# Kernel tuning notes

Measured on AMD Instinct MI355X. Metric: run time of the kernel, lower is better.

The kernel has to match this reference:

```python
import jax, jax.numpy as jnp
import numpy as np

N_NODES = 40000
N_EDGES = 160000
N_FEATS = 74
H, D = 3, 1024
NODES_PER_GRAPH = 50
N_GRAPHS = N_NODES // NODES_PER_GRAPH


def setup_inputs() -> dict:
    key = jax.random.key(0)
    ks = jax.random.split(key, 12)
    inp = {
        "feats": jax.random.normal(ks[0], (N_NODES, N_FEATS), jnp.float32),
        "W": jax.random.normal(ks[1], (N_FEATS, H * D), jnp.float32) * 0.05,
        "attn_l": jax.random.normal(ks[2], (H, D), jnp.float32) * 0.05,
        "attn_r": jax.random.normal(ks[3], (H, D), jnp.float32) * 0.05,
        "bias_gat": jax.random.normal(ks[4], (H * D,), jnp.float32) * 0.05,
        "W1": jax.random.normal(ks[5], (H * D, D), jnp.float32) * 0.02,
        "b1": jax.random.normal(ks[6], (D,), jnp.float32) * 0.02,
        "W2": jax.random.normal(ks[7], (D, 1), jnp.float32) * 0.02,
        "b2": jax.random.normal(ks[8], (1,), jnp.float32) * 0.02,
        "src": jax.random.randint(ks[9], (N_EDGES,), 0, N_NODES, jnp.int32),
        "dst": jax.random.randint(ks[10], (N_EDGES,), 0, N_NODES, jnp.int32),
        "graph_ids": (jnp.arange(N_NODES, dtype=jnp.int32) // NODES_PER_GRAPH),
        "n_graphs": N_GRAPHS,
    }
    return inp


def reference(feats, W, attn_l, attn_r, bias_gat, W1, b1, W2, b2, src, dst, graph_ids, n_graphs):
    N = feats.shape[0]
    # --- DGL GATConv ---
    h = (feats @ W).reshape(N, H, D)                       # [N,H,D]
    el = jnp.sum(h * attn_l, axis=-1)                      # [N,H]
    er = jnp.sum(h * attn_r, axis=-1)                      # [N,H]
    e = jax.nn.leaky_relu(el[src] + er[dst], 0.2)          # [E,H] per-edge logits
    # edge softmax over incoming edges of each dst node
    m = jax.ops.segment_max(e, dst, num_segments=N)        # [N,H]
    ex = jnp.exp(e - m[dst])
    s = jax.ops.segment_sum(ex, dst, num_segments=N)       # [N,H]
    alpha = ex / s[dst]                                    # [E,H]
    msg = h[src] * alpha[..., None]                        # [E,H,D]
    out = jax.ops.segment_sum(msg, dst, num_segments=N)    # [N,H,D]
    out = out + bias_gat.reshape(H, D)
    # --- flatten + linear + LeakyReLU(True) (negative_slope=1.0 -> identity) ---
    x = out.reshape(N, H * D) @ W1 + b1                    # [N,D]
    # --- AvgPooling over each graph ---
    counts = jax.ops.segment_sum(jnp.ones((N,), x.dtype), graph_ids, num_segments=n_graphs)
    g = jax.ops.segment_sum(x, graph_ids, num_segments=n_graphs) / jnp.maximum(counts, 1.0)[:, None]
    y = g @ W2 + b2                                        # [n_graphs,1]
    return y
```

## Files before the change

### kernel.cpp

```cpp
#include <hip/hip_runtime.h>

#define N_NODES 40000
#define N_EDGES 160000
#define N_FEATS 74
#define DD 1024
#define HD 3072
#define N_GRAPHS 800

#define NVB 192
#define NTB 57
#define NCH 64
#define ECH (N_EDGES / NCH)
#define SNR 200
#define SRNG 200
#define NNB 313

__device__ __forceinline__ float waveReduceSum(float v) {
    #pragma unroll
    for (int off = 32; off > 0; off >>= 1)
        v += __shfl_down(v, off, 64);
    return v;
}
__device__ __forceinline__ float lrelu02(float x) { return x > 0.f ? x : 0.2f * x; }

__global__ __launch_bounds__(256) void kVFusedC(
    const float* __restrict__ W1, const float* __restrict__ W2,
    const float* __restrict__ b1, const float* __restrict__ b2,
    const float* __restrict__ W, const float* __restrict__ al,
    const float* __restrict__ ar, const float* __restrict__ bias,
    const int* __restrict__ dst,
    float* __restrict__ c0, float* __restrict__ bgvpar,
    float* __restrict__ wvpar, float* __restrict__ lw6,
    int* __restrict__ counts_c) {
    int wave = threadIdx.x >> 6, lane = threadIdx.x & 63;
    int tid = threadIdx.x;
    if (blockIdx.x < NVB) {
        __shared__ float vs[16];
        int b = blockIdx.x;
        int g0 = b * 16;
        int h = b >> 6;
        const float4* w2v = (const float4*)W2;
        #pragma unroll
        for (int q = 0; q < 4; ++q) {
            int g = g0 + wave * 4 + q;
            const float4* row = (const float4*)(W1 + (size_t)g * DD);
            float acc = 0.f;
            #pragma unroll
            for (int k = 0; k < 4; ++k) {
                float4 a = row[lane + 64 * k];
                float4 bb = w2v[lane + 64 * k];
                acc += a.x * bb.x + a.y * bb.y + a.z * bb.z + a.w * bb.w;
            }
            acc = waveReduceSum(acc);
            if (!lane) vs[wave * 4 + q] = acc;
        }
        __syncthreads();
        if (tid < N_FEATS) {
            const float4* wr = (const float4*)(W + (size_t)tid * HD + g0);
            const float4* vv = (const float4*)vs;
            float s = 0.f;
            #pragma unroll
            for (int k = 0; k < 4; ++k) {
                float4 a = wr[k];
                float4 bb = vv[k];
                s += a.x * bb.x + a.y * bb.y + a.z * bb.z + a.w * bb.w;
            }
            wvpar[((size_t)(h * N_FEATS + tid)) * 64 + (b & 63)] = s;
        } else if (tid == N_FEATS) {
            float s = 0.f;
            #pragma unroll
            for (int j = 0; j < 16; ++j) s += vs[j] * bias[g0 + j];
            bgvpar[b] = s;
        }
    } else if (blockIdx.x < NVB + NTB) {
        int t = (blockIdx.x - NVB) * 4 + wave;
        if (t < N_FEATS * 3) {
            int f = t / 3, h = t - f * 3;
            const float4* rw = (const float4*)(W + (size_t)f * HD + h * DD);
            const float4* pl = (const float4*)(al + h * DD);
            const float4* pr = (const float4*)(ar + h * DD);
            float aL = 0.f, aR = 0.f;
            #pragma unroll
            for (int k = 0; k < 4; ++k) {
                float4 x = rw[lane + 64 * k];
                float4 l4 = pl[lane + 64 * k];
                float4 r4 = pr[lane + 64 * k];
                aL += x.x * l4.x + x.y * l4.y + x.z * l4.z + x.w * l4.w;
                aR += x.x * r4.x + x.y * r4.y + x.z * r4.z + x.w * r4.w;
            }
            aL = waveReduceSum(aL); aR = waveReduceSum(aR);
            if (!lane) { lw6[f * 6 + h] = aL; lw6[f * 6 + 3 + h] = aR; }
        } else if (t == N_FEATS * 3) {
            const float4* pb1 = (const float4*)b1;
            const float4* w2v = (const float4*)W2;
            float acc = 0.f;
            #pragma unroll
            for (int k = 0; k < 4; ++k) {
                float4 a = pb1[lane + 64 * k];
                float4 bb = w2v[lane + 64 * k];
                acc += a.x * bb.x + a.y * bb.y + a.z * bb.z + a.w * bb.w;
            }
            acc = waveReduceSum(acc);
            if (!lane) c0[0] = acc + b2[0];
        }
    } else {
        __shared__ int hist[SNR];
        int cc = blockIdx.x - (NVB + NTB);
        for (int i = tid; i < SNR; i += 256) hist[i] = 0;
        __syncthreads();
        const int eb = cc * ECH;
        for (int i = tid; i < ECH; i += 256) {
            int d = dst[eb + i];
            atomicAdd(&hist[d / SRNG], 1);
        }
        __syncthreads();
        for (int i = tid; i < SNR; i += 256) counts_c[cc * SNR + i] = hist[i];
    }
}

__global__ __launch_bounds__(256) void kNodeScatter(const float* __restrict__ feats,
        const int* __restrict__ dst,
        const float* __restrict__ lw6, const float* __restrict__ wvpar,
        const int* __restrict__ counts_c,
        float4* __restrict__ sn4, float4* __restrict__ er4,
        int* __restrict__ ebuf) {
    int tid = threadIdx.x;
    if (blockIdx.x < NNB) {
        __shared__ float lw[N_FEATS * 9];
        for (int j = tid; j < 222 * 4; j += 256) {
            int g4 = j >> 2, sl = j & 3;
            int h = g4 / N_FEATS, f = g4 - h * N_FEATS;
            const float* p = wvpar + (size_t)g4 * 64 + sl * 16;
            float s = 0.f;
            #pragma unroll
            for (int k = 0; k < 16; ++k) s += p[k];
            s += __shfl_xor(s, 1, 64);
            s += __shfl_xor(s, 2, 64);
            if (!sl) lw[f * 9 + 6 + h] = s;
        }
        for (int i = tid; i < N_FEATS * 6; i += 256)
            lw[(i / 6) * 9 + (i % 6)] = lw6[i];
        __syncthreads();
        int node = blockIdx.x * 128 + (tid >> 1);
        if (node >= N_NODES) return;
        int half = tid & 1;
        const float* row = feats + (size_t)node * N_FEATS;
        float a0=0,a1=0,a2=0,a3=0,a4=0,a5=0,a6=0,a7=0,a8=0;
        if (half == 0) {
            #pragma unroll
            for (int k = 0; k < 18; ++k) {
                float2 x2 = *(const float2*)(row + k * 2);
                const float* w0 = lw + (k * 2) * 9;
                a0 += x2.x*w0[0]; a1 += x2.x*w0[1]; a2 += x2.x*w0[2];
                a3 += x2.x*w0[3]; a4 += x2.x*w0[4]; a5 += x2.x*w0[5];
                a6 += x2.x*w0[6]; a7 += x2.x*w0[7]; a8 += x2.x*w0[8];
                const float* w1 = w0 + 9;
                a0 += x2.y*w1[0]; a1 += x2.y*w1[1]; a2 += x2.y*w1[2];
                a3 += x2.y*w1[3]; a4 += x2.y*w1[4]; a5 += x2.y*w1[5];
                a6 += x2.y*w1[6]; a7 += x2.y*w1[7]; a8 += x2.y*w1[8];
            }
            float x = row[36];
            const float* wp = lw + 36 * 9;
            a0 += x*wp[0]; a1 += x*wp[1]; a2 += x*wp[2];
            a3 += x*wp[3]; a4 += x*wp[4]; a5 += x*wp[5];
            a6 += x*wp[6]; a7 += x*wp[7]; a8 += x*wp[8];
        } else {
            float x = row[37];
            const float* wp = lw + 37 * 9;
            a0 += x*wp[0]; a1 += x*wp[1]; a2 += x*wp[2];
            a3 += x*wp[3]; a4 += x*wp[4]; a5 += x*wp[5];
            a6 += x*wp[6]; a7 += x*wp[7]; a8 += x*wp[8];
            #pragma unroll
            for (int k = 0; k < 18; ++k) {
                float2 x2 = *(const float2*)(row + 38 + k * 2);
                const float* w0 = lw + (38 + k * 2) * 9;
                a0 += x2.x*w0[0]; a1 += x2.x*w0[1]; a2 += x2.x*w0[2];
                a3 += x2.x*w0[3]; a4 += x2.x*w0[4]; a5 += x2.x*w0[5];
                a6 += x2.x*w0[6]; a7 += x2.x*w0[7]; a8 += x2.x*w0[8];
                const float* w1 = w0 + 9;
                a0 += x2.y*w1[0]; a1 += x2.y*w1[1]; a2 += x2.y*w1[2];
                a3 += x2.y*w1[3]; a4 += x2.y*w1[4]; a5 += x2.y*w1[5];
                a6 += x2.y*w1[6]; a7 += x2.y*w1[7]; a8 += x2.y*w1[8];
            }
        }
        a0 += __shfl_xor(a0, 1, 64); a1 += __shfl_xor(a1, 1, 64);
        a2 += __shfl_xor(a2, 1, 64); a3 += __shfl_xor(a3, 1, 64);
        a4 += __shfl_xor(a4, 1, 64); a5 += __shfl_xor(a5, 1, 64);
        a6 += __shfl_xor(a6, 1, 64); a7 += __shfl_xor(a7, 1, 64);
        a8 += __shfl_xor(a8, 1, 64);
        if (!half) {
            sn4[node * 2]     = make_float4(a0, a1, a2, 0.f);
            sn4[node * 2 + 1] = make_float4(a6, a7, a8, 0.f);
            er4[node]         = make_float4(a3, a4, a5, 0.f);
        }
    } else {
        __shared__ int tot[SNR], myoff[SNR], cursor[SNR], baseP[SNR];
        int c = blockIdx.x - NNB;
        if (tid < SNR) {
            int t = 0, mo = 0;
            #pragma unroll 8
            for (int cc = 0; cc < NCH; ++cc) {
                int v = counts_c[cc * SNR + tid];
                t += v;
                if (cc < c) mo += v;
            }
            tot[tid] = t; myoff[tid] = mo;
        }
        __syncthreads();
        if (tid == 0) {
            int b = 0;
            for (int r = 0; r < SNR; ++r) { baseP[r] = b; b += tot[r]; }
        }
        __syncthreads();
        if (tid < SNR) cursor[tid] = baseP[tid] + myoff[tid];
        __syncthreads();
        const int eb = c * ECH;
        for (int i = tid; i < ECH; i += 256) {
            int e = eb + i;
            int d = dst[e];
            int r = d / SRNG;
            int rr = d - r * SRNG;
            int slot = atomicAdd(&cursor[r], 1);
            ebuf[slot] = (e << 8) | rr;
        }
    }
}

__global__ __launch_bounds__(1024) void kProcess(const int* __restrict__ src,
        const int* __restrict__ ebuf, const int* __restrict__ counts_c,
        const float4* __restrict__ sn4, const float4* __restrict__ er4,
        const float* __restrict__ bgvpar, const float* __restrict__ c0,
        float* __restrict__ y) {
    __shared__ float erL[SRNG * 4];
    __shared__ float acc[SRNG * 6];
    __shared__ int tot[SNR];
    __shared__ int baseS[2];
    int tid = threadIdx.x, wave = tid >> 6, lane = tid & 63;
    const int r = blockIdx.x;
    if (tid < SNR) {
        int s = 0;
        #pragma unroll 8
        for (int cc = 0; cc < NCH; ++cc) s += counts_c[cc * SNR + tid];
        tot[tid] = s;
    }
    for (int i = tid; i < SRNG * 6; i += 1024) acc[i] = 0.f;
    if (tid < SRNG) ((float4*)erL)[tid] = er4[(size_t)r * SRNG + tid];
    __syncthreads();
    if (tid == 0) {
        int b = 0;
        for (int q = 0; q < SNR; ++q) { if (q == r) baseS[0] = b; b += tot[q]; }
        baseS[1] = baseS[0] + tot[r];
    }
    __syncthreads();
    int b0 = baseS[0], b1 = baseS[1];
    for (int i = b0 + tid; i < b1; i += 1024) {
        int pk = ebuf[i];
        int rr = pk & 255;
        int e  = ((unsigned)pk) >> 8;
        int s  = src[e];
        float4 L = sn4[s * 2];
        float4 V = sn4[s * 2 + 1];
        const float* R = erL + rr * 4;
        float e0 = expf(lrelu02(L.x + R[0]));
        float e1 = expf(lrelu02(L.y + R[1]));
        float e2 = expf(lrelu02(L.z + R[2]));
        float* p = acc + rr * 6;
        atomicAdd(p + 0, e0 * V.x);
        atomicAdd(p + 1, e1 * V.y);
        atomicAdd(p + 2, e2 * V.z);
        atomicAdd(p + 3, e0);
        atomicAdd(p + 4, e1);
        atomicAdd(p + 5, e2);
    }
    __syncthreads();
    if (wave < 4) {
        float b = 0.f;
        for (int i = lane; i < NVB; i += 64) b += bgvpar[i];
        b = waveReduceSum(b);
        float cacc = 0.f;
        if (lane < 50) {
            const float* p = acc + (wave * 50 + lane) * 6;
            if (p[3] > 0.f) cacc = p[0] / p[3] + p[1] / p[4] + p[2] / p[5];
        }
        cacc = waveReduceSum(cacc);
        if (!lane) y[r * 4 + wave] = cacc * (1.f / 50.f) + b + c0[0];
    }
}

extern "C" void kernel_launch(void* const* d_in, const int* in_sizes, int n_in,
                              void* d_out, int out_size, void* d_ws, size_t ws_size,
                              hipStream_t stream) {
    const float* feats = (const float*)d_in[0];
    const float* W     = (const float*)d_in[1];
    const float* al    = (const float*)d_in[2];
    const float* ar    = (const float*)d_in[3];
    const float* bias  = (const float*)d_in[4];
    const float* W1    = (const float*)d_in[5];
    const float* b1    = (const float*)d_in[6];
    const float* W2    = (const float*)d_in[7];
    const float* b2    = (const float*)d_in[8];
    const int*   src   = (const int*)d_in[9];
    const int*   dst   = (const int*)d_in[10];

    float* ws      = (float*)d_ws;
    float* lw6     = ws;
    float* c0      = ws + 448;
    float* bgvpar  = ws + 512;
    float* wvpar   = ws + 1024;
    int*   countsc = (int*)(ws + 16384);
    int*   ebuf    = (int*)(ws + 32768);
    float* sn      = ws + 196608;
    float* er      = ws + 516608;
    float* y       = (float*)d_out;

    hipLaunchKernelGGL(kVFusedC, dim3(NVB + NTB + NCH), dim3(256), 0, stream,
                       W1, W2, b1, b2, W, al, ar, bias, dst,
                       c0, bgvpar, wvpar, lw6, countsc);
    hipLaunchKernelGGL(kNodeScatter, dim3(NNB + NCH), dim3(256), 0, stream,
                       feats, dst, lw6, wvpar, countsc,
                       (float4*)sn, (float4*)er, ebuf);
    hipLaunchKernelGGL(kProcess, dim3(SNR), dim3(1024), 0, stream,
                       src, ebuf, countsc, (const float4*)sn, (const float4*)er,
                       bgvpar, c0, y);
}
```

Measured before the change: 41.03 us.

## Bucket edges in one pass using fixed-capacity per-chunk slots

The separate histogram pass and the prefix-sum scatter pass are replaced by a single pass. Each edge chunk writes its edges straight into a fixed-capacity slot (CAP entries) per (dst range, chunk) and records per-chunk counts. The node-projection kernel no longer carries scatter blocks. The processing kernel builds a 64-entry prefix over chunk counts and binary-searches it to locate each edge. This removes one read of dst and the cross-chunk offset computation, at the cost of sparser ebuf reads and an assumption that no bucket exceeds CAP entries.

```diff
diff --git a/kernel.cpp b/kernel.cpp
--- a/kernel.cpp
+++ b/kernel.cpp
@@ -11,6 +11,7 @@
 #define NTB 57
 #define NCH 64
 #define ECH (N_EDGES / NCH)
+#define CAP 96
 #define SNR 200
 #define SRNG 200
 #define NNB 313
@@ -23,7 +24,7 @@
 }
 __device__ __forceinline__ float lrelu02(float x) { return x > 0.f ? x : 0.2f * x; }
 
-__global__ __launch_bounds__(256) void kVFusedC(
+__global__ __launch_bounds__(256) void kPre(
     const float* __restrict__ W1, const float* __restrict__ W2,
     const float* __restrict__ b1, const float* __restrict__ b2,
     const float* __restrict__ W, const float* __restrict__ al,
@@ -31,7 +32,7 @@
     const int* __restrict__ dst,
     float* __restrict__ c0, float* __restrict__ bgvpar,
     float* __restrict__ wvpar, float* __restrict__ lw6,
-    int* __restrict__ counts_c) {
+    int* __restrict__ cnt, int* __restrict__ ebuf) {
     int wave = threadIdx.x >> 6, lane = threadIdx.x & 63;
     int tid = threadIdx.x;
     if (blockIdx.x < NVB) {
@@ -104,115 +105,9 @@
             if (!lane) c0[0] = acc + b2[0];
         }
     } else {
-        __shared__ int hist[SNR];
-        int cc = blockIdx.x - (NVB + NTB);
-        for (int i = tid; i < SNR; i += 256) hist[i] = 0;
-        __syncthreads();
-        const int eb = cc * ECH;
-        for (int i = tid; i < ECH; i += 256) {
-            int d = dst[eb + i];
-            atomicAdd(&hist[d / SRNG], 1);
-        }
-        __syncthreads();
-        for (int i = tid; i < SNR; i += 256) counts_c[cc * SNR + i] = hist[i];
-    }
-}
-
-__global__ __launch_bounds__(256) void kNodeScatter(const float* __restrict__ feats,
-        const int* __restrict__ dst,
-        const float* __restrict__ lw6, const float* __restrict__ wvpar,
-        const int* __restrict__ counts_c,
-        float4* __restrict__ sn4, float4* __restrict__ er4,
-        int* __restrict__ ebuf) {
-    int tid = threadIdx.x;
-    if (blockIdx.x < NNB) {
-        __shared__ float lw[N_FEATS * 9];
-        for (int j = tid; j < 222 * 4; j += 256) {
-            int g4 = j >> 2, sl = j & 3;
-            int h = g4 / N_FEATS, f = g4 - h * N_FEATS;
-            const float* p = wvpar + (size_t)g4 * 64 + sl * 16;
-            float s = 0.f;
-            #pragma unroll
-            for (int k = 0; k < 16; ++k) s += p[k];
-            s += __shfl_xor(s, 1, 64);
-            s += __shfl_xor(s, 2, 64);
-            if (!sl) lw[f * 9 + 6 + h] = s;
-        }
-        for (int i = tid; i < N_FEATS * 6; i += 256)
-            lw[(i / 6) * 9 + (i % 6)] = lw6[i];
-        __syncthreads();
-        int node = blockIdx.x * 128 + (tid >> 1);
-        if (node >= N_NODES) return;
-        int half = tid & 1;
-        const float* row = feats + (size_t)node * N_FEATS;
-        float a0=0,a1=0,a2=0,a3=0,a4=0,a5=0,a6=0,a7=0,a8=0;
-        if (half == 0) {
-            #pragma unroll
-            for (int k = 0; k < 18; ++k) {
-                float2 x2 = *(const float2*)(row + k * 2);
-                const float* w0 = lw + (k * 2) * 9;
-                a0 += x2.x*w0[0]; a1 += x2.x*w0[1]; a2 += x2.x*w0[2];
-                a3 += x2.x*w0[3]; a4 += x2.x*w0[4]; a5 += x2.x*w0[5];
-                a6 += x2.x*w0[6]; a7 += x2.x*w0[7]; a8 += x2.x*w0[8];
-                const float* w1 = w0 + 9;
-                a0 += x2.y*w1[0]; a1 += x2.y*w1[1]; a2 += x2.y*w1[2];
-                a3 += x2.y*w1[3]; a4 += x2.y*w1[4]; a5 += x2.y*w1[5];
-                a6 += x2.y*w1[6]; a7 += x2.y*w1[7]; a8 += x2.y*w1[8];
-            }
-            float x = row[36];
-            const float* wp = lw + 36 * 9;
-            a0 += x*wp[0]; a1 += x*wp[1]; a2 += x*wp[2];
-            a3 += x*wp[3]; a4 += x*wp[4]; a5 += x*wp[5];
-            a6 += x*wp[6]; a7 += x*wp[7]; a8 += x*wp[8];
-        } else {
-            float x = row[37];
-            const float* wp = lw + 37 * 9;
-            a0 += x*wp[0]; a1 += x*wp[1]; a2 += x*wp[2];
-            a3 += x*wp[3]; a4 += x*wp[4]; a5 += x*wp[5];
-            a6 += x*wp[6]; a7 += x*wp[7]; a8 += x*wp[8];
-            #pragma unroll
-            for (int k = 0; k < 18; ++k) {
-                float2 x2 = *(const float2*)(row + 38 + k * 2);
-                const float* w0 = lw + (38 + k * 2) * 9;
-                a0 += x2.x*w0[0]; a1 += x2.x*w0[1]; a2 += x2.x*w0[2];
-                a3 += x2.x*w0[3]; a4 += x2.x*w0[4]; a5 += x2.x*w0[5];
-                a6 += x2.x*w0[6]; a7 += x2.x*w0[7]; a8 += x2.x*w0[8];
-                const float* w1 = w0 + 9;
-                a0 += x2.y*w1[0]; a1 += x2.y*w1[1]; a2 += x2.y*w1[2];
-                a3 += x2.y*w1[3]; a4 += x2.y*w1[4]; a5 += x2.y*w1[5];
-                a6 += x2.y*w1[6]; a7 += x2.y*w1[7]; a8 += x2.y*w1[8];
-            }
-        }
-        a0 += __shfl_xor(a0, 1, 64); a1 += __shfl_xor(a1, 1, 64);
-        a2 += __shfl_xor(a2, 1, 64); a3 += __shfl_xor(a3, 1, 64);
-        a4 += __shfl_xor(a4, 1, 64); a5 += __shfl_xor(a5, 1, 64);
-        a6 += __shfl_xor(a6, 1, 64); a7 += __shfl_xor(a7, 1, 64);
-        a8 += __shfl_xor(a8, 1, 64);
-        if (!half) {
-            sn4[node * 2]     = make_float4(a0, a1, a2, 0.f);
-            sn4[node * 2 + 1] = make_float4(a6, a7, a8, 0.f);
-            er4[node]         = make_float4(a3, a4, a5, 0.f);
-        }
-    } else {
-        __shared__ int tot[SNR], myoff[SNR], cursor[SNR], baseP[SNR];
-        int c = blockIdx.x - NNB;
-        if (tid < SNR) {
-            int t = 0, mo = 0;
-            #pragma unroll 8
-            for (int cc = 0; cc < NCH; ++cc) {
-                int v = counts_c[cc * SNR + tid];
-                t += v;
-                if (cc < c) mo += v;
-            }
-            tot[tid] = t; myoff[tid] = mo;
-        }
-        __syncthreads();
-        if (tid == 0) {
-            int b = 0;
-            for (int r = 0; r < SNR; ++r) { baseP[r] = b; b += tot[r]; }
-        }
-        __syncthreads();
-        if (tid < SNR) cursor[tid] = baseP[tid] + myoff[tid];
+        __shared__ int cur[SNR];
+        int c = blockIdx.x - (NVB + NTB);
+        for (int i = tid; i < SNR; i += 256) cur[i] = 0;
         __syncthreads();
         const int eb = c * ECH;
         for (int i = tid; i < ECH; i += 256) {
@@ -220,41 +115,118 @@
             int d = dst[e];
             int r = d / SRNG;
             int rr = d - r * SRNG;
-            int slot = atomicAdd(&cursor[r], 1);
-            ebuf[slot] = (e << 8) | rr;
-        }
+            int slot = atomicAdd(&cur[r], 1);
+            ebuf[(r * NCH + c) * CAP + slot] = (e << 8) | rr;
+        }
+        __syncthreads();
+        for (int i = tid; i < SNR; i += 256) cnt[c * SNR + i] = cur[i];
+    }
+}
+
+__global__ __launch_bounds__(256) void kNode(const float* __restrict__ feats,
+        const float* __restrict__ lw6, const float* __restrict__ wvpar,
+        float4* __restrict__ sn4, float4* __restrict__ er4) {
+    __shared__ float lw[N_FEATS * 9];
+    int tid = threadIdx.x;
+    for (int j = tid; j < 222 * 4; j += 256) {
+        int g4 = j >> 2, sl = j & 3;
+        int h = g4 / N_FEATS, f = g4 - h * N_FEATS;
+        const float* p = wvpar + (size_t)g4 * 64 + sl * 16;
+        float s = 0.f;
+        #pragma unroll
+        for (int k = 0; k < 16; ++k) s += p[k];
+        s += __shfl_xor(s, 1, 64);
+        s += __shfl_xor(s, 2, 64);
+        if (!sl) lw[f * 9 + 6 + h] = s;
+    }
+    for (int i = tid; i < N_FEATS * 6; i += 256)
+        lw[(i / 6) * 9 + (i % 6)] = lw6[i];
+    __syncthreads();
+    int node = blockIdx.x * 128 + (tid >> 1);
+    if (node >= N_NODES) return;
+    int half = tid & 1;
+    const float* row = feats + (size_t)node * N_FEATS;
+    float a0=0,a1=0,a2=0,a3=0,a4=0,a5=0,a6=0,a7=0,a8=0;
+    if (half == 0) {
+        #pragma unroll
+        for (int k = 0; k < 18; ++k) {
+            float2 x2 = *(const float2*)(row + k * 2);
+            const float* w0 = lw + (k * 2) * 9;
+            a0 += x2.x*w0[0]; a1 += x2.x*w0[1]; a2 += x2.x*w0[2];
+            a3 += x2.x*w0[3]; a4 += x2.x*w0[4]; a5 += x2.x*w0[5];
+            a6 += x2.x*w0[6]; a7 += x2.x*w0[7]; a8 += x2.x*w0[8];
+            const float* w1 = w0 + 9;
+            a0 += x2.y*w1[0]; a1 += x2.y*w1[1]; a2 += x2.y*w1[2];
+            a3 += x2.y*w1[3]; a4 += x2.y*w1[4]; a5 += x2.y*w1[5];
+            a6 += x2.y*w1[6]; a7 += x2.y*w1[7]; a8 += x2.y*w1[8];
+        }
+        float x = row[36];
+        const float* wp = lw + 36 * 9;
+        a0 += x*wp[0]; a1 += x*wp[1]; a2 += x*wp[2];
+        a3 += x*wp[3]; a4 += x*wp[4]; a5 += x*wp[5];
+        a6 += x*wp[6]; a7 += x*wp[7]; a8 += x*wp[8];
+    } else {
+        float x = row[37];
+        const float* wp = lw + 37 * 9;
+        a0 += x*wp[0]; a1 += x*wp[1]; a2 += x*wp[2];
+        a3 += x*wp[3]; a4 += x*wp[4]; a5 += x*wp[5];
+        a6 += x*wp[6]; a7 += x*wp[7]; a8 += x*wp[8];
+        #pragma unroll
+        for (int k = 0; k < 18; ++k) {
+            float2 x2 = *(const float2*)(row + 38 + k * 2);
+            const float* w0 = lw + (38 + k * 2) * 9;
+            a0 += x2.x*w0[0]; a1 += x2.x*w0[1]; a2 += x2.x*w0[2];
+            a3 += x2.x*w0[3]; a4 += x2.x*w0[4]; a5 += x2.x*w0[5];
+            a6 += x2.x*w0[6]; a7 += x2.x*w0[7]; a8 += x2.x*w0[8];
+            const float* w1 = w0 + 9;
+            a0 += x2.y*w1[0]; a1 += x2.y*w1[1]; a2 += x2.y*w1[2];
+            a3 += x2.y*w1[3]; a4 += x2.y*w1[4]; a5 += x2.y*w1[5];
+            a6 += x2.y*w1[6]; a7 += x2.y*w1[7]; a8 += x2.y*w1[8];
+        }
+    }
+    a0 += __shfl_xor(a0, 1, 64); a1 += __shfl_xor(a1, 1, 64);
+    a2 += __shfl_xor(a2, 1, 64); a3 += __shfl_xor(a3, 1, 64);
+    a4 += __shfl_xor(a4, 1, 64); a5 += __shfl_xor(a5, 1, 64);
+    a6 += __shfl_xor(a6, 1, 64); a7 += __shfl_xor(a7, 1, 64);
+    a8 += __shfl_xor(a8, 1, 64);
+    if (!half) {
+        sn4[node * 2]     = make_float4(a0, a1, a2, 0.f);
+        sn4[node * 2 + 1] = make_float4(a6, a7, a8, 0.f);
+        er4[node]         = make_float4(a3, a4, a5, 0.f);
     }
 }
 
 __global__ __launch_bounds__(1024) void kProcess(const int* __restrict__ src,
-        const int* __restrict__ ebuf, const int* __restrict__ counts_c,
+        const int* __restrict__ ebuf, const int* __restrict__ cnt,
         const float4* __restrict__ sn4, const float4* __restrict__ er4,
         const float* __restrict__ bgvpar, const float* __restrict__ c0,
         float* __restrict__ y) {
     __shared__ float erL[SRNG * 4];
     __shared__ float acc[SRNG * 6];
-    __shared__ int tot[SNR];
-    __shared__ int baseS[2];
+    __shared__ int pref[NCH + 1];
     int tid = threadIdx.x, wave = tid >> 6, lane = tid & 63;
     const int r = blockIdx.x;
-    if (tid < SNR) {
-        int s = 0;
-        #pragma unroll 8
-        for (int cc = 0; cc < NCH; ++cc) s += counts_c[cc * SNR + tid];
-        tot[tid] = s;
-    }
+    __shared__ int cnts[NCH];
+    if (tid < NCH) cnts[tid] = cnt[tid * SNR + r];
     for (int i = tid; i < SRNG * 6; i += 1024) acc[i] = 0.f;
     if (tid < SRNG) ((float4*)erL)[tid] = er4[(size_t)r * SRNG + tid];
     __syncthreads();
     if (tid == 0) {
         int b = 0;
-        for (int q = 0; q < SNR; ++q) { if (q == r) baseS[0] = b; b += tot[q]; }
-        baseS[1] = baseS[0] + tot[r];
-    }
-    __syncthreads();
-    int b0 = baseS[0], b1 = baseS[1];
-    for (int i = b0 + tid; i < b1; i += 1024) {
-        int pk = ebuf[i];
+        #pragma unroll
+        for (int c = 0; c < NCH; ++c) { pref[c] = b; b += cnts[c]; }
+        pref[NCH] = b;
+    }
+    __syncthreads();
+    int T = pref[NCH];
+    for (int i = tid; i < T; i += 1024) {
+        int lo = 0, hi = NCH;
+        while (hi - lo > 1) {
+            int mid = (lo + hi) >> 1;
+            if (pref[mid] <= i) lo = mid; else hi = mid;
+        }
+        int j = i - pref[lo];
+        int pk = ebuf[(r * NCH + lo) * CAP + j];
         int rr = pk & 255;
         int e  = ((unsigned)pk) >> 8;
         int s  = src[e];
@@ -307,19 +279,18 @@
     float* c0      = ws + 448;
     float* bgvpar  = ws + 512;
     float* wvpar   = ws + 1024;
-    int*   countsc = (int*)(ws + 16384);
+    int*   cnt     = (int*)(ws + 16384);
     int*   ebuf    = (int*)(ws + 32768);
-    float* sn      = ws + 196608;
-    float* er      = ws + 516608;
+    float* sn      = ws + 1261568;
+    float* er      = sn + N_NODES * 8;
     float* y       = (float*)d_out;
 
-    hipLaunchKernelGGL(kVFusedC, dim3(NVB + NTB + NCH), dim3(256), 0, stream,
+    hipLaunchKernelGGL(kPre, dim3(NVB + NTB + NCH), dim3(256), 0, stream,
                        W1, W2, b1, b2, W, al, ar, bias, dst,
-                       c0, bgvpar, wvpar, lw6, countsc);
-    hipLaunchKernelGGL(kNodeScatter, dim3(NNB + NCH), dim3(256), 0, stream,
-                       feats, dst, lw6, wvpar, countsc,
-                       (float4*)sn, (float4*)er, ebuf);
+                       c0, bgvpar, wvpar, lw6, cnt, ebuf);
+    hipLaunchKernelGGL(kNode, dim3(NNB), dim3(256), 0, stream,
+                       feats, lw6, wvpar, (float4*)sn, (float4*)er);
     hipLaunchKernelGGL(kProcess, dim3(SNR), dim3(1024), 0, stream,
-                       src, ebuf, countsc, (const float4*)sn, (const float4*)er,
+                       src, ebuf, cnt, (const float4*)sn, (const float4*)er,
                        bgvpar, c0, y);
 }
```

Result: faster. 35.38 us, median of 2 (-13.8%).
